# Performance work log

Hardware: AMD Instinct MI355X
Metric: run time of the kernel (lower is better)

Reference implementation:

```python
import jax, jax.numpy as jnp
import numpy as np

N, E, F, HID, OUT, B, HEADS = 4096, 131072, 64, 64, 86, 16, 4


def setup_inputs() -> dict:
    key = jax.random.key(0)
    ks = jax.random.split(key, 12)
    s = 0.1
    return {
        "x": jax.random.normal(ks[0], (N, F), dtype=jnp.float32),
        "edge_index": jax.random.randint(ks[1], (2, E), 0, N),
        "edge_attr": jax.random.uniform(ks[2], (E,), dtype=jnp.float32),
        "batch": jnp.sort(jax.random.randint(ks[3], (N,), 0, B)).astype(jnp.int32),
        # GCNConv1: Linear(F -> HID, no bias) + post-aggregation bias
        "W1": jax.random.normal(ks[4], (HID, F), dtype=jnp.float32) * s,
        "b1": jnp.zeros((HID,), jnp.float32),
        # MultiheadAttention(embed_dim=HID, num_heads=4)
        "Win": jax.random.normal(ks[5], (3 * HID, HID), dtype=jnp.float32) * s,
        "b_in": jnp.zeros((3 * HID,), jnp.float32),
        "Wout": jax.random.normal(ks[6], (HID, HID), dtype=jnp.float32) * s,
        "b_out": jnp.zeros((HID,), jnp.float32),
        # GCNConv2: Linear(HID -> OUT)
        "W2": jax.random.normal(ks[7], (OUT, HID), dtype=jnp.float32) * s,
        "b2": jnp.zeros((OUT,), jnp.float32),
    }


def _gcn_layer(h, W, b, src_a, dst_a, norm, n):
    # x' = scatter_add(norm * (x W^T)[src] -> dst) + b   (PyG GCNConv)
    h = h @ W.T
    agg = jax.ops.segment_sum(norm[:, None] * h[src_a], dst_a, num_segments=n)
    return agg + b


def reference(x, edge_index, edge_attr, batch, W1, b1, Win, b_in, Wout, b_out, W2, b2):
    n = x.shape[0]
    # torch.cat([x[:, :-1], x[:, -1:].view(-1,1)], dim=1) == x (identity)
    src, dst = edge_index[0], edge_index[1]
    loop = jnp.arange(n)
    src_a = jnp.concatenate([src, loop])
    dst_a = jnp.concatenate([dst, loop])
    w_a = jnp.concatenate([edge_attr, jnp.ones((n,), x.dtype)])  # self-loops weight 1
    deg = jax.ops.segment_sum(w_a, dst_a, num_segments=n)
    dis = jnp.where(deg > 0, jax.lax.rsqrt(jnp.maximum(deg, 1e-12)), 0.0)
    norm = dis[src_a] * w_a * dis[dst_a]

    h = jax.nn.relu(_gcn_layer(x, W1, b1, src_a, dst_a, norm, n))  # [N, HID]

    # MultiheadAttention over the whole node set as one sequence (batch=1)
    qkv = h @ Win.T + b_in
    q, k, v = jnp.split(qkv, 3, axis=-1)
    dh = HID // HEADS
    to_heads = lambda t: t.reshape(n, HEADS, dh).transpose(1, 0, 2)  # [H, N, dh]
    q, k, v = to_heads(q), to_heads(k), to_heads(v)
    scores = jnp.einsum("hnd,hmd->hnm", q, k) * (1.0 / np.sqrt(dh))
    att = jax.nn.softmax(scores, axis=-1)
    o = jnp.einsum("hnm,hmd->hnd", att, v).transpose(1, 0, 2).reshape(n, HID)
    o = o @ Wout.T + b_out

    h2 = _gcn_layer(o, W2, b2, src_a, dst_a, norm, n)  # [N, OUT]

    # global_mean_pool over graph ids
    sums = jax.ops.segment_sum(h2, batch, num_segments=B)
    cnt = jax.ops.segment_sum(jnp.ones((n,), h2.dtype), batch, num_segments=B)
    return sums / jnp.maximum(cnt, 1.0)[:, None]
```

## Files before the change

### kernel.cpp

```cpp
#include <hip/hip_runtime.h>

constexpr int N = 4096, E = 131072, OUTF = 86, NB = 16, HEADS = 4, DH = 16;
constexpr int CAP = 128;
constexpr int NSPLIT = 8, KEYS = N / NSPLIT;
constexpr int PCKS = 8;

typedef __attribute__((ext_vector_type(8))) short short8;
typedef __attribute__((ext_vector_type(4))) float f32x4;

constexpr unsigned long long PK_MASK = (1ULL << 40) - 1;
constexpr float PK_SCALE = 1.0f / 16777216.0f;

constexpr size_t OFF_PCK   = 0;
constexpr size_t OFF_INV   = OFF_PCK + 16 * (size_t)N;
constexpr size_t OFF_BUFA  = OFF_INV + 16;
constexpr size_t OFF_QP    = OFF_BUFA + (size_t)N * 64;
constexpr size_t OFF_KP    = OFF_QP + (size_t)N * 32;
constexpr size_t OFF_VP    = OFF_KP + (size_t)N * 32;
constexpr size_t OFF_H2    = OFF_VP + (size_t)N * 32;
constexpr size_t OFF_EPAIR = OFF_H2 + (size_t)N * 86;
constexpr size_t OFF_NORMV = OFF_EPAIR + (size_t)2 * N * CAP;
constexpr size_t OFF_OPART = OFF_NORMV + (size_t)N * CAP;
constexpr size_t OFF_LPART = OFF_OPART + (size_t)HEADS * N * NSPLIT * 16;

__device__ inline unsigned short f2bf(float f) {
    unsigned u = __builtin_bit_cast(unsigned, f);
    u += 0x7FFFu + ((u >> 16) & 1u);
    return (unsigned short)(u >> 16);
}

__device__ inline float pk_deg(unsigned long long pk) {
    return (float)(pk & PK_MASK) * PK_SCALE;
}

__global__ __launch_bounds__(256) void d1_kernel(const float* __restrict__ x,
        const float* __restrict__ W1, const int* __restrict__ ei,
        const float* __restrict__ ea, const int* __restrict__ batch,
        const float* __restrict__ b2, float* __restrict__ ws, float* __restrict__ out) {
    __shared__ float4 Ws4[64 * 17];
    __shared__ float4 As4[16 * 17];
    __shared__ int bnd[NB + 1];
    int blk = blockIdx.x, tid = threadIdx.x;
    if (blk < 256) {
        float* bufA = ws + OFF_BUFA;
        for (int idx = tid; idx < 64 * 16; idx += 256)
            Ws4[(idx >> 4) * 17 + (idx & 15)] = ((const float4*)W1)[idx];
        {
            int r = tid >> 4, k4 = tid & 15;
            As4[r * 17 + k4] = ((const float4*)x)[(size_t)(blk * 16 + r) * 16 + k4];
        }
        __syncthreads();
        int r2 = tid & 7, cg = tid >> 3;
        float acc[2][2] = {};
#pragma unroll
        for (int k4 = 0; k4 < 16; ++k4) {
            float4 a0 = As4[r2 * 17 + k4], a1 = As4[(r2 + 8) * 17 + k4];
#pragma unroll
            for (int i = 0; i < 2; ++i) {
                float4 w = Ws4[(cg + 32 * i) * 17 + k4];
                acc[0][i] += a0.x * w.x + a0.y * w.y + a0.z * w.z + a0.w * w.w;
                acc[1][i] += a1.x * w.x + a1.y * w.y + a1.z * w.z + a1.w * w.w;
            }
        }
#pragma unroll
        for (int j = 0; j < 2; ++j)
#pragma unroll
            for (int i = 0; i < 2; ++i)
                bufA[(size_t)(blk * 16 + r2 + 8 * j) * 64 + cg + 32 * i] = acc[j][i];
    } else if (blk < 512) {
        unsigned long long* pck = (unsigned long long*)(ws + OFF_PCK);
        int2* epair = (int2*)(ws + OFF_EPAIR);
        int f = (blk - 256) * 256 + tid;
        int e0 = f, e1 = f + E / 2;
        int s0 = ei[e0], d0 = ei[E + e0];
        int s1 = ei[e1], d1 = ei[E + e1];
        float w0 = ea[e0], w1 = ea[e1];
        unsigned long long a0 = (1ULL << 40) + (unsigned long long)(unsigned)(w0 * 16777216.0f + 0.5f);
        unsigned long long a1 = (1ULL << 40) + (unsigned long long)(unsigned)(w1 * 16777216.0f + 0.5f);
        unsigned long long o0 = atomicAdd(&pck[(size_t)d0 * PCKS], a0);
        unsigned long long o1 = atomicAdd(&pck[(size_t)d1 * PCKS], a1);
        int p0 = (int)(o0 >> 40), p1 = (int)(o1 >> 40);
        if (p0 < CAP) epair[(size_t)d0 * CAP + p0] = make_int2(s0, __float_as_int(w0));
        if (p1 < CAP) epair[(size_t)d1 * CAP + p1] = make_int2(s1, __float_as_int(w1));
    } else {
        float* invcnt = ws + OFF_INV;
        if (tid <= NB) {
            int b = tid, lo = 0, hi = N;
            while (lo < hi) { int m = (lo + hi) >> 1; if (batch[m] < b) lo = m + 1; else hi = m; }
            bnd[tid] = lo;
        }
        __syncthreads();
        if (tid < NB) {
            int cnt = bnd[tid + 1] - bnd[tid];
            invcnt[tid] = cnt > 0 ? 1.0f / (float)cnt : 0.0f;
        }
        for (int idx = tid; idx < NB * OUTF; idx += 256) {
            int b = idx / OUTF;
            int cnt = bnd[b + 1] - bnd[b];
            out[idx] = cnt > 0 ? b2[idx - b * OUTF] : 0.0f;
        }
    }
}

__global__ __launch_bounds__(1024) void d23_kernel(const float* __restrict__ Win,
        const float* __restrict__ b1, const float* __restrict__ b_in,
        float* __restrict__ ws) {
    __shared__ float4 Ws4[16 * 200];
    __shared__ float  Af[16 * 68];

    const unsigned long long* pck = (const unsigned long long*)(ws + OFF_PCK);
    const int2*  epair = (const int2*)(ws + OFF_EPAIR);
    float*       normv = ws + OFF_NORMV;
    const float* bufA  = ws + OFF_BUFA;
    unsigned short* Qp = (unsigned short*)(ws + OFF_QP);
    unsigned short* Kp = (unsigned short*)(ws + OFF_KP);
    unsigned short* Vp = (unsigned short*)(ws + OFF_VP);

    const int tid = threadIdx.x, lane = tid & 63, wv = tid >> 6;
    for (int idx = tid; idx < 192 * 16; idx += 1024) {
        int c = idx >> 4, k4 = idx & 15;
        Ws4[k4 * 200 + c] = ((const float4*)Win)[idx];
    }

    const int node = blockIdx.x * 16 + wv;
    {
        const unsigned long long pkn = pck[(size_t)node * PCKS];
        const float di = rsqrtf(pk_deg(pkn) + 1.0f);
        float acc0 = (di * di) * bufA[(size_t)node * 64 + lane];
        float acc1 = 0.f, acc2 = 0.f, acc3 = 0.f;
        const int cnt = min((int)(pkn >> 40), CAP);
        const int2* pe = epair + (size_t)node * CAP;
        for (int base = 0; base < cnt; base += 64) {
            int rem = cnt - base;
            int   sl = 0;
            float nl = 0.f;
            if (lane < rem) {
                int2 e = pe[base + lane];
                sl = e.x;
                float w = __int_as_float(e.y);
                nl = rsqrtf(pk_deg(pck[(size_t)sl * PCKS]) + 1.0f) * w * di;
                normv[(size_t)node * CAP + base + lane] = nl;
            }
            int m = rem < 64 ? rem : 64;
            int j = 0;
            for (; j + 4 <= m; j += 4) {
                int   s0 = __shfl(sl, j),     s1 = __shfl(sl, j + 1);
                int   s2 = __shfl(sl, j + 2), s3 = __shfl(sl, j + 3);
                float n0 = __shfl(nl, j),     n1 = __shfl(nl, j + 1);
                float n2 = __shfl(nl, j + 2), n3 = __shfl(nl, j + 3);
                acc0 += n0 * bufA[(size_t)s0 * 64 + lane];
                acc1 += n1 * bufA[(size_t)s1 * 64 + lane];
                acc2 += n2 * bufA[(size_t)s2 * 64 + lane];
                acc3 += n3 * bufA[(size_t)s3 * 64 + lane];
            }
            for (; j < m; ++j) {
                int   s0 = __shfl(sl, j);
                float n0 = __shfl(nl, j);
                acc0 += n0 * bufA[(size_t)s0 * 64 + lane];
            }
        }
        Af[wv * 68 + lane] = fmaxf((acc0 + acc1) + (acc2 + acc3) + b1[lane], 0.0f);
    }
    __syncthreads();

    {
        const float4* Af4 = (const float4*)Af;
        float acc[3];
#pragma unroll
        for (int i = 0; i < 3; ++i) acc[i] = b_in[lane + 64 * i];
#pragma unroll
        for (int k4 = 0; k4 < 16; ++k4) {
            float4 a = Af4[wv * 17 + k4];
#pragma unroll
            for (int i = 0; i < 3; ++i) {
                float4 w = Ws4[k4 * 200 + lane + 64 * i];
                acc[i] += a.x * w.x + a.y * w.y + a.z * w.z + a.w * w.w;
            }
        }
        const int row = node;
#pragma unroll
        for (int i = 0; i < 3; ++i) {
            int c = lane + 64 * i;
            float v = acc[i];
            if (c < 64) {
                int h = c >> 4, d = c & 15;
                Qp[((size_t)h * N + row) * 16 + d] = f2bf(v * 0.25f);
            } else if (c < 128) {
                int c2 = c - 64, h = c2 >> 4, d = c2 & 15;
                Kp[((size_t)h * N + row) * 16 + d] = f2bf(v);
            } else {
                int c2 = c - 128, h = c2 >> 4, d = c2 & 15;
                Vp[((size_t)h * 16 + d) * N + row] = f2bf(v);
            }
        }
    }
}

__global__ __launch_bounds__(256) void attn_kernel(const float* __restrict__ ws_c,
        float* __restrict__ ws) {
    __shared__ __align__(16) unsigned short Plds[4 * 640];

    const unsigned short* Qp = (const unsigned short*)(ws_c + OFF_QP);
    const unsigned short* Kp = (const unsigned short*)(ws_c + OFF_KP);
    const unsigned short* Vp = (const unsigned short*)(ws_c + OFF_VP);
    float* opart = ws + OFF_OPART;
    float* lpart = ws + OFF_LPART;

    const int h  = blockIdx.y;
    const int sp = blockIdx.z;
    const int k0 = sp * KEYS;
    const int tid = threadIdx.x;
    const int lane = tid & 63, wv = tid >> 6;
    const int q15 = lane & 15, quad = lane >> 4;

    const int qbase = blockIdx.x * 64 + wv * 16;
    short8 qf = {};
    if (quad < 2)
        qf = *(const short8*)&Qp[((size_t)h * N + qbase + q15) * 16 + quad * 8];

    f32x4 O = {0.f, 0.f, 0.f, 0.f};
    float l = 0.f;
    unsigned short* Pw = &Plds[wv * 640];
    const unsigned short* Kh = Kp + (size_t)h * N * 16;
    const unsigned short* Vh = Vp + ((size_t)h * 16 + q15) * N + k0;

#pragma unroll 2
    for (int ch = 0; ch < KEYS / 32; ++ch) {
#pragma unroll
        for (int t = 0; t < 2; ++t) {
            short8 kf = {};
            if (quad < 2)
                kf = *(const short8*)&Kh[(size_t)(k0 + ch * 32 + t * 16 + q15) * 16 + quad * 8];
            f32x4 zero = {0.f, 0.f, 0.f, 0.f};
            f32x4 s = __builtin_amdgcn_mfma_f32_16x16x32_bf16(kf, qf, zero, 0, 0, 0);
            float p0 = __expf(s[0]), p1 = __expf(s[1]), p2 = __expf(s[2]), p3 = __expf(s[3]);
            l += p0 + p1 + p2 + p3;
            ushort4 pu;
            pu.x = f2bf(p0); pu.y = f2bf(p1); pu.z = f2bf(p2); pu.w = f2bf(p3);
            *(ushort4*)&Pw[q15 * 40 + t * 16 + quad * 4] = pu;
        }
        asm volatile("s_waitcnt lgkmcnt(0)" ::: "memory");
        short8 pf = *(const short8*)&Pw[q15 * 40 + quad * 8];
        short8 vf = *(const short8*)&Vh[ch * 32 + quad * 8];
        O = __builtin_amdgcn_mfma_f32_16x16x32_bf16(pf, vf, O, 0, 0, 0);
    }

    l += __shfl_xor(l, 16);
    l += __shfl_xor(l, 32);
    if (lane < 16)
        lpart[((size_t)h * N + qbase + q15) * NSPLIT + sp] = l;
#pragma unroll
    for (int r = 0; r < 4; ++r) {
        int query = qbase + quad * 4 + r;
        opart[(((size_t)h * N + query) * NSPLIT + sp) * 16 + q15] = O[r];
    }
}

__global__ __launch_bounds__(256) void d4b_kernel(const float* __restrict__ Wout,
        const float* __restrict__ b_out, const float* __restrict__ W2,
        float* __restrict__ ws) {
    __shared__ float4 WoS[64 * 17];
    __shared__ float4 W2S[96 * 17];
    __shared__ float  o_sh[16 * 68];
    __shared__ float  Bf[16 * 68];

    const float* opart = ws + OFF_OPART;
    const float* lpart = ws + OFF_LPART;
    float* h2pre = ws + OFF_H2;

    const int tid = threadIdx.x, qbase = blockIdx.x * 16;
    for (int idx = tid; idx < 64 * 16; idx += 256)
        WoS[(idx >> 4) * 17 + (idx & 15)] = ((const float4*)Wout)[idx];
    for (int idx = tid; idx < 86 * 16; idx += 256)
        W2S[(idx >> 4) * 17 + (idx & 15)] = ((const float4*)W2)[idx];

    for (int idx = tid; idx < 16 * 64; idx += 256) {
        int r = idx >> 6, f = idx & 63;
        int h = f >> 4, d = f & 15;
        size_t base = ((size_t)h * N + qbase + r) * NSPLIT;
        float L = 0.f, acc = 0.f;
#pragma unroll
        for (int s = 0; s < NSPLIT; ++s) {
            L += lpart[base + s];
            acc += opart[(base + s) * 16 + d];
        }
        o_sh[r * 68 + f] = acc / L;
    }
    __syncthreads();
    {
        int r = tid & 15, c0 = tid >> 4;
        float4* o4 = (float4*)o_sh;
#pragma unroll
        for (int i = 0; i < 4; ++i) {
            int c = c0 + 16 * i;
            float acc = b_out[c];
#pragma unroll
            for (int k4 = 0; k4 < 16; ++k4) {
                float4 a = o4[r * 17 + k4];
                float4 w = WoS[c * 17 + k4];
                acc += a.x * w.x + a.y * w.y + a.z * w.z + a.w * w.w;
            }
            Bf[r * 68 + c] = acc;
        }
    }
    __syncthreads();
    {
        int r = tid & 15, c0 = tid >> 4;
        float4* B4 = (float4*)Bf;
#pragma unroll
        for (int i = 0; i < 6; ++i) {
            int c = c0 + 16 * i;
            if (c < OUTF) {
                float acc = 0.f;
#pragma unroll
                for (int k4 = 0; k4 < 16; ++k4) {
                    float4 a = B4[r * 17 + k4];
                    float4 w = W2S[c * 17 + k4];
                    acc += a.x * w.x + a.y * w.y + a.z * w.z + a.w * w.w;
                }
                h2pre[(size_t)(qbase + r) * OUTF + c] = acc;
            }
        }
    }
}

__global__ __launch_bounds__(1024) void d5_kernel(const int* __restrict__ batch,
        float* __restrict__ ws, float* __restrict__ out) {
    __shared__ float vec[16][88];
    __shared__ int   bix[16];

    const unsigned long long* pck = (const unsigned long long*)(ws + OFF_PCK);
    const int2*  epair = (const int2*)(ws + OFF_EPAIR);
    const float* normv = ws + OFF_NORMV;
    const float* invcnt= ws + OFF_INV;
    const float* h2pre = ws + OFF_H2;

    const int tid = threadIdx.x;
    const int lane = tid & 63, wv = tid >> 6;
    const int node = blockIdx.x * 16 + wv;
    const bool hi2 = lane < (OUTF - 64);
    const int b = batch[node];
    const float inv = invcnt[b];
    const unsigned long long pkn = pck[(size_t)node * PCKS];
    const float di2 = 1.0f / (pk_deg(pkn) + 1.0f);
    const float* Hn = h2pre + (size_t)node * OUTF;
    float a0 = di2 * Hn[lane],                  a1 = 0.f, a2 = 0.f, a3 = 0.f;
    float c0 = hi2 ? di2 * Hn[64 + lane] : 0.f, c1 = 0.f, c2 = 0.f, c3 = 0.f;
    const int cnt = min((int)(pkn >> 40), CAP);
    const int2* pe = epair + (size_t)node * CAP;

    for (int base = 0; base < cnt; base += 64) {
        int rem = cnt - base;
        int   sl = 0;
        float nl = 0.f;
        if (lane < rem) {
            sl = pe[base + lane].x;
            nl = normv[(size_t)node * CAP + base + lane];
        }
        int m = rem < 64 ? rem : 64;
        int j = 0;
        for (; j + 4 <= m; j += 4) {
            int   s0 = __shfl(sl, j),     s1 = __shfl(sl, j + 1);
            int   s2 = __shfl(sl, j + 2), s3 = __shfl(sl, j + 3);
            float n0 = __shfl(nl, j),     n1 = __shfl(nl, j + 1);
            float n2 = __shfl(nl, j + 2), n3 = __shfl(nl, j + 3);
            const float* H0 = h2pre + (size_t)s0 * OUTF;
            const float* H1 = h2pre + (size_t)s1 * OUTF;
            const float* H2 = h2pre + (size_t)s2 * OUTF;
            const float* H3 = h2pre + (size_t)s3 * OUTF;
            a0 += n0 * H0[lane]; if (hi2) c0 += n0 * H0[64 + lane];
            a1 += n1 * H1[lane]; if (hi2) c1 += n1 * H1[64 + lane];
            a2 += n2 * H2[lane]; if (hi2) c2 += n2 * H2[64 + lane];
            a3 += n3 * H3[lane]; if (hi2) c3 += n3 * H3[64 + lane];
        }
        for (; j < m; ++j) {
            int   s0 = __shfl(sl, j);
            float n0 = __shfl(nl, j);
            const float* H0 = h2pre + (size_t)s0 * OUTF;
            a0 += n0 * H0[lane];
            if (hi2) c0 += n0 * H0[64 + lane];
        }
    }
    vec[wv][lane] = ((a0 + a1) + (a2 + a3)) * inv;
    if (hi2) vec[wv][64 + lane] = ((c0 + c1) + (c2 + c3)) * inv;
    if (lane == 0) bix[wv] = b;
    __syncthreads();
    if (tid < OUTF) {
        int curb = bix[0];
        float acc = 0.f;
#pragma unroll
        for (int w = 0; w < 16; ++w) {
            int bw = bix[w];
            if (bw != curb) {
                atomicAdd(&out[curb * OUTF + tid], acc);
                curb = bw; acc = 0.f;
            }
            acc += vec[w][tid];
        }
        atomicAdd(&out[curb * OUTF + tid], acc);
    }
}

extern "C" void kernel_launch(void* const* d_in, const int* in_sizes, int n_in,
                              void* d_out, int out_size, void* d_ws, size_t ws_size,
                              hipStream_t stream) {
    const float* x     = (const float*)d_in[0];
    const int*   ei    = (const int*)  d_in[1];
    const float* ea    = (const float*)d_in[2];
    const int*   batch = (const int*)  d_in[3];
    const float* W1    = (const float*)d_in[4];
    const float* b1    = (const float*)d_in[5];
    const float* Win   = (const float*)d_in[6];
    const float* b_in  = (const float*)d_in[7];
    const float* Wout  = (const float*)d_in[8];
    const float* b_out = (const float*)d_in[9];
    const float* W2    = (const float*)d_in[10];
    const float* b2    = (const float*)d_in[11];
    float* out = (float*)d_out;
    float* ws  = (float*)d_ws;

    hipMemsetAsync(ws + OFF_PCK, 0, (size_t)N * 64, stream);
    d1_kernel<<<513, 256, 0, stream>>>(x, W1, ei, ea, batch, b2, ws, out);
    d23_kernel<<<N / 16, 1024, 0, stream>>>(Win, b1, b_in, ws);
    attn_kernel<<<dim3(N / 64, HEADS, NSPLIT), 256, 0, stream>>>(ws, ws);
    d4b_kernel<<<N / 16, 256, 0, stream>>>(Wout, b_out, W2, ws);
    d5_kernel<<<N / 16, 1024, 0, stream>>>(batch, ws, out);
}
```

Measured before the change: 154.4 us.

## Halve attention key splits, add 8-way gather unroll, setprio around MFMAs, packed bf16 convert

Reduces the attention key-split count from 8 to 4, so each wave processes twice as many keys and there are fewer partial outputs to combine. Adds an 8-wide unrolled gather loop to both GCN aggregation kernels so more independent loads are in flight. Wraps the MFMA instructions in s_setprio and replaces the scalar bf16 rounding with a packed two-value conversion. The lower split count cuts the number of attention waves, which may reduce occupancy and latency hiding.

```diff
diff --git a/kernel.cpp b/kernel.cpp
--- a/kernel.cpp
+++ b/kernel.cpp
@@ -1,8 +1,9 @@
 #include <hip/hip_runtime.h>
+#include <hip/hip_bf16.h>
 
 constexpr int N = 4096, E = 131072, OUTF = 86, NB = 16, HEADS = 4, DH = 16;
 constexpr int CAP = 128;
-constexpr int NSPLIT = 8, KEYS = N / NSPLIT;
+constexpr int NSPLIT = 4, KEYS = N / NSPLIT;
 constexpr int PCKS = 8;
 
 typedef __attribute__((ext_vector_type(8))) short short8;
@@ -27,6 +28,13 @@
     unsigned u = __builtin_bit_cast(unsigned, f);
     u += 0x7FFFu + ((u >> 16) & 1u);
     return (unsigned short)(u >> 16);
+}
+
+__device__ inline unsigned pk2bf(float a, float b) {
+    __hip_bfloat162 h2 = __float22bfloat162_rn(make_float2(a, b));
+    union { __hip_bfloat162 h; unsigned u; } c;
+    c.h = h2;
+    return c.u;
 }
 
 __device__ inline float pk_deg(unsigned long long pk) {
@@ -143,6 +151,22 @@
             }
             int m = rem < 64 ? rem : 64;
             int j = 0;
+            for (; j + 8 <= m; j += 8) {
+                int   s0 = __shfl(sl, j),     s1 = __shfl(sl, j + 1);
+                int   s2 = __shfl(sl, j + 2), s3 = __shfl(sl, j + 3);
+                int   s4 = __shfl(sl, j + 4), s5 = __shfl(sl, j + 5);
+                int   s6 = __shfl(sl, j + 6), s7 = __shfl(sl, j + 7);
+                float n0 = __shfl(nl, j),     n1 = __shfl(nl, j + 1);
+                float n2 = __shfl(nl, j + 2), n3 = __shfl(nl, j + 3);
+                float n4 = __shfl(nl, j + 4), n5 = __shfl(nl, j + 5);
+                float n6 = __shfl(nl, j + 6), n7 = __shfl(nl, j + 7);
+                float v0 = bufA[(size_t)s0 * 64 + lane], v1 = bufA[(size_t)s1 * 64 + lane];
+                float v2 = bufA[(size_t)s2 * 64 + lane], v3 = bufA[(size_t)s3 * 64 + lane];
+                float v4 = bufA[(size_t)s4 * 64 + lane], v5 = bufA[(size_t)s5 * 64 + lane];
+                float v6 = bufA[(size_t)s6 * 64 + lane], v7 = bufA[(size_t)s7 * 64 + lane];
+                acc0 += n0 * v0; acc1 += n1 * v1; acc2 += n2 * v2; acc3 += n3 * v3;
+                acc0 += n4 * v4; acc1 += n5 * v5; acc2 += n6 * v6; acc3 += n7 * v7;
+            }
             for (; j + 4 <= m; j += 4) {
                 int   s0 = __shfl(sl, j),     s1 = __shfl(sl, j + 1);
                 int   s2 = __shfl(sl, j + 2), s3 = __shfl(sl, j + 3);
@@ -232,17 +256,22 @@
             if (quad < 2)
                 kf = *(const short8*)&Kh[(size_t)(k0 + ch * 32 + t * 16 + q15) * 16 + quad * 8];
             f32x4 zero = {0.f, 0.f, 0.f, 0.f};
+            __builtin_amdgcn_s_setprio(1);
             f32x4 s = __builtin_amdgcn_mfma_f32_16x16x32_bf16(kf, qf, zero, 0, 0, 0);
+            __builtin_amdgcn_s_setprio(0);
             float p0 = __expf(s[0]), p1 = __expf(s[1]), p2 = __expf(s[2]), p3 = __expf(s[3]);
-            l += p0 + p1 + p2 + p3;
-            ushort4 pu;
-            pu.x = f2bf(p0); pu.y = f2bf(p1); pu.z = f2bf(p2); pu.w = f2bf(p3);
-            *(ushort4*)&Pw[q15 * 40 + t * 16 + quad * 4] = pu;
+            l += (p0 + p1) + (p2 + p3);
+            uint2 pk;
+            pk.x = pk2bf(p0, p1);
+            pk.y = pk2bf(p2, p3);
+            *(uint2*)&Pw[q15 * 40 + t * 16 + quad * 4] = pk;
         }
         asm volatile("s_waitcnt lgkmcnt(0)" ::: "memory");
         short8 pf = *(const short8*)&Pw[q15 * 40 + quad * 8];
         short8 vf = *(const short8*)&Vh[ch * 32 + quad * 8];
+        __builtin_amdgcn_s_setprio(1);
         O = __builtin_amdgcn_mfma_f32_16x16x32_bf16(pf, vf, O, 0, 0, 0);
+        __builtin_amdgcn_s_setprio(0);
     }
 
     l += __shfl_xor(l, 16);
@@ -359,6 +388,36 @@
         }
         int m = rem < 64 ? rem : 64;
         int j = 0;
+        for (; j + 8 <= m; j += 8) {
+            int   s0 = __shfl(sl, j),     s1 = __shfl(sl, j + 1);
+            int   s2 = __shfl(sl, j + 2), s3 = __shfl(sl, j + 3);
+            int   s4 = __shfl(sl, j + 4), s5 = __shfl(sl, j + 5);
+            int   s6 = __shfl(sl, j + 6), s7 = __shfl(sl, j + 7);
+            float n0 = __shfl(nl, j),     n1 = __shfl(nl, j + 1);
+            float n2 = __shfl(nl, j + 2), n3 = __shfl(nl, j + 3);
+            float n4 = __shfl(nl, j + 4), n5 = __shfl(nl, j + 5);
+            float n6 = __shfl(nl, j + 6), n7 = __shfl(nl, j + 7);
+            const float* H0 = h2pre + (size_t)s0 * OUTF;
+            const float* H1 = h2pre + (size_t)s1 * OUTF;
+            const float* H2 = h2pre + (size_t)s2 * OUTF;
+            const float* H3 = h2pre + (size_t)s3 * OUTF;
+            const float* H4 = h2pre + (size_t)s4 * OUTF;
+            const float* H5 = h2pre + (size_t)s5 * OUTF;
+            const float* H6 = h2pre + (size_t)s6 * OUTF;
+            const float* H7 = h2pre + (size_t)s7 * OUTF;
+            float v0 = H0[lane], v1 = H1[lane], v2 = H2[lane], v3 = H3[lane];
+            float v4 = H4[lane], v5 = H5[lane], v6 = H6[lane], v7 = H7[lane];
+            a0 += n0 * v0; a1 += n1 * v1; a2 += n2 * v2; a3 += n3 * v3;
+            a0 += n4 * v4; a1 += n5 * v5; a2 += n6 * v6; a3 += n7 * v7;
+            if (hi2) {
+                float w0 = H0[64 + lane], w1 = H1[64 + lane];
+                float w2 = H2[64 + lane], w3 = H3[64 + lane];
+                float w4 = H4[64 + lane], w5 = H5[64 + lane];
+                float w6 = H6[64 + lane], w7 = H7[64 + lane];
+                c0 += n0 * w0; c1 += n1 * w1; c2 += n2 * w2; c3 += n3 * w3;
+                c0 += n4 * w4; c1 += n5 * w5; c2 += n6 * w6; c3 += n7 * w7;
+            }
+        }
         for (; j + 4 <= m; j += 4) {
             int   s0 = __shfl(sl, j),     s1 = __shfl(sl, j + 1);
             int   s2 = __shfl(sl, j + 2), s3 = __shfl(sl, j + 3);
```

Result: no change. 155.0 us (+0.3%).
